# Optimization experiments

Hardware: AMD Instinct MI355X
Metric: run time of the kernel (lower is better)

Reference implementation:

```python
import jax, jax.numpy as jnp
import numpy as np

POOL = 7  # pool_size from init


def _crop_and_resize_one(fm, boxes):
    """TF crop_and_resize semantics for one image.
    fm: [H,W,C] float; boxes: [N,4] normalized x1y1x2y2 (module reorders to y1x1y2x2
    before calling tf.image.crop_and_resize; here we just pick the right coords).
    Returns [N,POOL,POOL,C]."""
    H, W, C = fm.shape
    x1, y1, x2, y2 = boxes[:, 0], boxes[:, 1], boxes[:, 2], boxes[:, 3]
    i = jnp.arange(POOL, dtype=fm.dtype)
    # sample coords per TF: start*(size-1) + i*(end-start)*(size-1)/(POOL-1)
    ys = y1[:, None] * (H - 1) + i[None, :] * ((y2 - y1) * (H - 1) / (POOL - 1))[:, None]  # [N,P]
    xs = x1[:, None] * (W - 1) + i[None, :] * ((x2 - x1) * (W - 1) / (POOL - 1))[:, None]  # [N,P]

    def lerp_idx(v, size):
        v0 = jnp.floor(v)
        frac = v - v0
        i0 = jnp.clip(v0, 0, size - 1).astype(jnp.int32)
        i1 = jnp.clip(v0 + 1, 0, size - 1).astype(jnp.int32)
        valid = (v >= 0) & (v <= size - 1)  # TF extrapolates with 0 outside image
        return i0, i1, frac, valid

    yt, yb, fy, vy = lerp_idx(ys, H)
    xl, xr, fx, vx = lerp_idx(xs, W)
    # gather 4 corners via advanced indexing -> [N,P,P,C]
    tl = fm[yt[:, :, None], xl[:, None, :]]
    tr = fm[yt[:, :, None], xr[:, None, :]]
    bl = fm[yb[:, :, None], xl[:, None, :]]
    br = fm[yb[:, :, None], xr[:, None, :]]
    fy_ = fy[:, :, None, None]
    fx_ = fx[:, None, :, None]
    top = tl + (tr - tl) * fx_
    bot = bl + (br - bl) * fx_
    out = top + (bot - top) * fy_
    mask = (vy[:, :, None] & vx[:, None, :])[..., None]
    return jnp.where(mask, out, jnp.zeros((), fm.dtype))


def setup_inputs() -> dict:
    key = jax.random.key(0)
    k1, k2, k3 = jax.random.split(key, 3)
    B, H, W, C, N = 8, 64, 64, 256, 512
    feature_map = jax.random.normal(k1, (B, H, W, C), dtype=jnp.float32)
    # build valid normalized boxes x1y1x2y2 with x1<=x2, y1<=y2
    p = jax.random.uniform(k2, (B, N, 2), dtype=jnp.float32)
    q = jax.random.uniform(k3, (B, N, 2), dtype=jnp.float32)
    lo = jnp.minimum(p, q)
    hi = jnp.maximum(p, q)
    rpn_pred = jnp.concatenate([lo, hi], axis=-1)  # [B,N,4] x1y1x2y2
    return {"feature_map": feature_map, "rpn_pred": rpn_pred}


def reference(feature_map, rpn_pred):
    # vmap over batch replaces the tf.while_loop over images
    return jax.vmap(_crop_and_resize_one)(feature_map, rpn_pred)  # [B,N,P,P,C]
```

## Files before the change

kernel.cpp:

```cpp
#include <hip/hip_runtime.h>


#define POOL  7
#define B_    8
#define H_    64
#define W_    64
#define C_    256
#define N_    512
#define CW    (C_ / 4)
#define ROWS_PER_IMG (N_ * POOL)
#define ROWS_PER_BLOCK 4

typedef float v4f __attribute__((ext_vector_type(4)));

__global__ __launch_bounds__(256) void roialign_kernel(
    const float* __restrict__ fm,
    const float* __restrict__ boxes,
    float* __restrict__ out)
{
    const int b    = blockIdx.x & 7;
    const int rblk = blockIdx.x >> 3;
    const int wave = threadIdx.x >> 6;
    const int lane = threadIdx.x & 63;
    const int row  = rblk * ROWS_PER_BLOCK + wave;
    const int n    = row / POOL;
    const int py   = row - n * POOL;

    const float* box = boxes + ((b << 9) + n) * 4;
    const float bx1 = box[0], by1 = box[1], bx2 = box[2], by2 = box[3];

    const float sy  = (by2 - by1) * 63.0f / 6.0f;
    const float sx  = (bx2 - bx1) * 63.0f / 6.0f;
    const float yv  = by1 * 63.0f + (float)py * sy;
    const float x0v = bx1 * 63.0f;

    const float yf = floorf(yv);
    const float fy = yv - yf;
    const int   y0 = (int)yf;
    const int   yt = min(max(y0,     0), H_ - 1);
    const int   yb = min(max(y0 + 1, 0), H_ - 1);
    const bool  vy = (yv >= 0.0f) && (yv <= 63.0f);

    const v4f* f4  = (const v4f*)fm;
    const int rowT = (b * (H_ * W_) + yt * W_) * CW + lane;
    const int rowB = (b * (H_ * W_) + yb * W_) * CW + lane;

    v4f* o4 = (v4f*)out + ((((b << 9) + n) * POOL + py) * POOL) * CW + lane;

    #pragma unroll
    for (int px = 0; px < POOL; ++px) {
        const float xv = x0v + (float)px * sx;
        const float xf = floorf(xv);
        const float fx = xv - xf;
        const int   x0 = (int)xf;
        const int   xl = min(max(x0,     0), W_ - 1);
        const int   xr = min(max(x0 + 1, 0), W_ - 1);
        const bool  valid = vy && (xv >= 0.0f) && (xv <= 63.0f);

        const v4f tl = f4[rowT + xl * CW];
        const v4f tr = f4[rowT + xr * CW];
        const v4f bl = f4[rowB + xl * CW];
        const v4f br = f4[rowB + xr * CW];

        const v4f top = tl + (tr - tl) * fx;
        const v4f bot = bl + (br - bl) * fx;
        v4f o = top + (bot - top) * fy;
        if (!valid) o = (v4f)(0.0f);

        __builtin_nontemporal_store(o, o4 + px * CW);
    }
}

extern "C" void kernel_launch(void* const* d_in, const int* in_sizes, int n_in,
                              void* d_out, int out_size, void* d_ws, size_t ws_size,
                              hipStream_t stream) {
    const float* fm    = (const float*)d_in[0];
    const float* boxes = (const float*)d_in[1];
    float* out         = (float*)d_out;

    const int blocks = (ROWS_PER_IMG / ROWS_PER_BLOCK) * B_;

    roialign_kernel<<<blocks, 256, 0, stream>>>(fm, boxes, out);
}
```

Baseline: 246.0 us.

## Sort boxes by y1 per image to improve feature-map cache locality

Adds a per-image bitonic sort of box indices by y1 coordinate in shared memory, then has the RoI-align kernel process boxes in sorted order via a permutation array. Neighbouring blocks then touch similar feature-map rows, with the aim of raising L2/MALL hit rates on the gathers. Output is still written to each box's original slot, so results are unchanged. The cost is an extra small kernel launch, a workspace dependency and a serialized dependent load of the permutation. Writes become scattered by box rather than sequential.

```diff
diff --git a/kernel.cpp b/kernel.cpp
--- a/kernel.cpp
+++ b/kernel.cpp
@@ -13,9 +13,38 @@
 
 typedef float v4f __attribute__((ext_vector_type(4)));
 
+__global__ __launch_bounds__(512) void sort_boxes_kernel(
+    const float* __restrict__ boxes,
+    int* __restrict__ perm)
+{
+    const int b = blockIdx.x;
+    const int t = threadIdx.x;
+    __shared__ float key[N_];
+    __shared__ int   idx[N_];
+    key[t] = boxes[((b << 9) + t) * 4 + 1];
+    idx[t] = t;
+    __syncthreads();
+    for (int k = 2; k <= N_; k <<= 1) {
+        for (int j = k >> 1; j > 0; j >>= 1) {
+            const int ixj = t ^ j;
+            if (ixj > t) {
+                const bool up = ((t & k) == 0);
+                const float a = key[t], c = key[ixj];
+                if (up ? (a > c) : (a < c)) {
+                    key[t] = c; key[ixj] = a;
+                    const int tmp = idx[t]; idx[t] = idx[ixj]; idx[ixj] = tmp;
+                }
+            }
+            __syncthreads();
+        }
+    }
+    perm[(b << 9) + t] = idx[t];
+}
+
 __global__ __launch_bounds__(256) void roialign_kernel(
     const float* __restrict__ fm,
     const float* __restrict__ boxes,
+    const int*  __restrict__ perm,
     float* __restrict__ out)
 {
     const int b    = blockIdx.x & 7;
@@ -23,8 +52,10 @@
     const int wave = threadIdx.x >> 6;
     const int lane = threadIdx.x & 63;
     const int row  = rblk * ROWS_PER_BLOCK + wave;
-    const int n    = row / POOL;
-    const int py   = row - n * POOL;
+    const int ns   = row / POOL;
+    const int py   = row - ns * POOL;
+
+    const int n = __builtin_amdgcn_readfirstlane(perm[(b << 9) + ns]);
 
     const float* box = boxes + ((b << 9) + n) * 4;
     const float bx1 = box[0], by1 = box[1], bx2 = box[2], by2 = box[3];
@@ -77,8 +108,10 @@
     const float* fm    = (const float*)d_in[0];
     const float* boxes = (const float*)d_in[1];
     float* out         = (float*)d_out;
+    int*   perm        = (int*)d_ws;
+
+    sort_boxes_kernel<<<B_, N_, 0, stream>>>(boxes, perm);
 
     const int blocks = (ROWS_PER_IMG / ROWS_PER_BLOCK) * B_;
-
-    roialign_kernel<<<blocks, 256, 0, stream>>>(fm, boxes, out);
+    roialign_kernel<<<blocks, 256, 0, stream>>>(fm, boxes, perm, out);
 }
```

After: 259.1 us. +5.3%, slower.

## Bucket ROI sample rows by feature-map row and serve bilinear taps from LDS

Applied to the files above, without the earlier changes.

Adds a pre-pass kernel that builds, per image, a histogram and prefix sum that group every (box, pool-row) item by the top feature-map row it samples. The main kernel then runs one block per (image, row). Each block stages that row and the row below (128 KB) in LDS and processes all bucketed items, reading the four bilinear corners from LDS instead of global memory. This is meant to remove repeated scattered global/L2 gathers. In exchange it adds a second launch and a serial scan, and drops to 512 blocks with very large LDS use, which limits occupancy. Bucket sizes are uneven, so blocks get unequal work, and the large dynamic LDS request may need hardware and launch support.

```diff
diff --git a/kernel.cpp b/kernel.cpp
--- a/kernel.cpp
+++ b/kernel.cpp
@@ -8,66 +8,129 @@
 #define C_    256
 #define N_    512
 #define CW    (C_ / 4)
-#define ROWS_PER_IMG (N_ * POOL)
-#define ROWS_PER_BLOCK 4
+#define ROWQ  (W_ * CW)
+#define ITEMS_PER_IMG (N_ * POOL)
 
 typedef float v4f __attribute__((ext_vector_type(4)));
+typedef unsigned short u16;
+
+__global__ __launch_bounds__(512) void bucket_kernel(
+    const float* __restrict__ boxes,
+    int* __restrict__ offs,
+    u16* __restrict__ items)
+{
+    const int b = blockIdx.x;
+    const int n = threadIdx.x;
+    __shared__ int hist[H_];
+    __shared__ int base[H_];
+    __shared__ int cnt[H_];
+    if (n < H_) hist[n] = 0;
+    __syncthreads();
+
+    const float by1 = boxes[(((b << 9) + n) << 2) + 1];
+    const float by2 = boxes[(((b << 9) + n) << 2) + 3];
+    const float sy = (by2 - by1) * 63.0f / 6.0f;
+    int bk[POOL];
+    #pragma unroll
+    for (int py = 0; py < POOL; ++py) {
+        const float yv = by1 * 63.0f + (float)py * sy;
+        const int y0 = (int)floorf(yv);
+        bk[py] = min(max(y0, 0), H_ - 1);
+        atomicAdd(&hist[bk[py]], 1);
+    }
+    __syncthreads();
+    if (n == 0) {
+        int run = 0;
+        for (int i = 0; i < H_; ++i) { base[i] = run; run += hist[i]; }
+    }
+    if (n < H_) cnt[n] = 0;
+    __syncthreads();
+    #pragma unroll
+    for (int py = 0; py < POOL; ++py) {
+        const int pos = base[bk[py]] + atomicAdd(&cnt[bk[py]], 1);
+        items[b * ITEMS_PER_IMG + pos] = (u16)((n << 3) | py);
+    }
+    if (n < H_) offs[b * (H_ + 1) + n] = base[n];
+    if (n == 0) offs[b * (H_ + 1) + H_] = ITEMS_PER_IMG;
+}
 
 __global__ __launch_bounds__(256) void roialign_kernel(
     const float* __restrict__ fm,
     const float* __restrict__ boxes,
+    const int*  __restrict__ offs,
+    const u16*  __restrict__ items,
     float* __restrict__ out)
 {
+    extern __shared__ v4f lds[];
     const int b    = blockIdx.x & 7;
-    const int rblk = blockIdx.x >> 3;
-    const int wave = threadIdx.x >> 6;
-    const int lane = threadIdx.x & 63;
-    const int row  = rblk * ROWS_PER_BLOCK + wave;
-    const int n    = row / POOL;
-    const int py   = row - n * POOL;
+    const int bk   = blockIdx.x >> 3;
+    const int tid  = threadIdx.x;
+    const int wave = tid >> 6;
+    const int lane = tid & 63;
+    const v4f* f4  = (const v4f*)fm;
 
-    const float* box = boxes + ((b << 9) + n) * 4;
-    const float bx1 = box[0], by1 = box[1], bx2 = box[2], by2 = box[3];
+    {
+        const int base0 = (b * H_ + bk) * ROWQ;
+        const int base1 = (b * H_ + min(bk + 1, H_ - 1)) * ROWQ;
+        #pragma unroll
+        for (int k = 0; k < 16; ++k)
+            lds[k * 256 + tid] = f4[base0 + k * 256 + tid];
+        #pragma unroll
+        for (int k = 0; k < 16; ++k)
+            lds[ROWQ + k * 256 + tid] = f4[base1 + k * 256 + tid];
+    }
+    __syncthreads();
 
-    const float sy  = (by2 - by1) * 63.0f / 6.0f;
-    const float sx  = (bx2 - bx1) * 63.0f / 6.0f;
-    const float yv  = by1 * 63.0f + (float)py * sy;
-    const float x0v = bx1 * 63.0f;
+    const int start = offs[b * (H_ + 1) + bk];
+    const int end   = offs[b * (H_ + 1) + bk + 1];
 
-    const float yf = floorf(yv);
-    const float fy = yv - yf;
-    const int   y0 = (int)yf;
-    const int   yt = min(max(y0,     0), H_ - 1);
-    const int   yb = min(max(y0 + 1, 0), H_ - 1);
-    const bool  vy = (yv >= 0.0f) && (yv <= 63.0f);
+    for (int it = start + wave; it < end; it += 4) {
+        const int code = __builtin_amdgcn_readfirstlane(
+                             (int)items[b * ITEMS_PER_IMG + it]);
+        const int n  = code >> 3;
+        const int py = code & 7;
 
-    const v4f* f4  = (const v4f*)fm;
-    const int rowT = (b * (H_ * W_) + yt * W_) * CW + lane;
-    const int rowB = (b * (H_ * W_) + yb * W_) * CW + lane;
+        const float* box = boxes + (((b << 9) + n) << 2);
+        const float bx1 = box[0], by1 = box[1], bx2 = box[2], by2 = box[3];
 
-    v4f* o4 = (v4f*)out + ((((b << 9) + n) * POOL + py) * POOL) * CW + lane;
+        const float sy  = (by2 - by1) * 63.0f / 6.0f;
+        const float sx  = (bx2 - bx1) * 63.0f / 6.0f;
+        const float yv  = by1 * 63.0f + (float)py * sy;
+        const float x0v = bx1 * 63.0f;
 
-    #pragma unroll
-    for (int px = 0; px < POOL; ++px) {
-        const float xv = x0v + (float)px * sx;
-        const float xf = floorf(xv);
-        const float fx = xv - xf;
-        const int   x0 = (int)xf;
-        const int   xl = min(max(x0,     0), W_ - 1);
-        const int   xr = min(max(x0 + 1, 0), W_ - 1);
-        const bool  valid = vy && (xv >= 0.0f) && (xv <= 63.0f);
+        const float yf = floorf(yv);
+        const float fy = yv - yf;
+        const int   y0 = (int)yf;
+        const int   yt = min(max(y0,     0), H_ - 1);
+        const int   yb = min(max(y0 + 1, 0), H_ - 1);
+        const bool  vy = (yv >= 0.0f) && (yv <= 63.0f);
 
-        const v4f tl = f4[rowT + xl * CW];
-        const v4f tr = f4[rowT + xr * CW];
-        const v4f bl = f4[rowB + xl * CW];
-        const v4f br = f4[rowB + xr * CW];
+        const int offB = (yb > yt) ? ROWQ : 0;
 
-        const v4f top = tl + (tr - tl) * fx;
-        const v4f bot = bl + (br - bl) * fx;
-        v4f o = top + (bot - top) * fy;
-        if (!valid) o = (v4f)(0.0f);
+        v4f* o4 = (v4f*)out + ((((b << 9) + n) * POOL + py) * POOL) * CW + lane;
 
-        __builtin_nontemporal_store(o, o4 + px * CW);
+        #pragma unroll
+        for (int px = 0; px < POOL; ++px) {
+            const float xv = x0v + (float)px * sx;
+            const float xf = floorf(xv);
+            const float fx = xv - xf;
+            const int   x0 = (int)xf;
+            const int   xl = min(max(x0,     0), W_ - 1);
+            const int   xr = min(max(x0 + 1, 0), W_ - 1);
+            const bool  valid = vy && (xv >= 0.0f) && (xv <= 63.0f);
+
+            const v4f tl = lds[       xl * CW + lane];
+            const v4f tr = lds[       xr * CW + lane];
+            const v4f bl = lds[offB + xl * CW + lane];
+            const v4f br = lds[offB + xr * CW + lane];
+
+            const v4f top = tl + (tr - tl) * fx;
+            const v4f bot = bl + (br - bl) * fx;
+            v4f o = top + (bot - top) * fy;
+            if (!valid) o = (v4f)(0.0f);
+
+            __builtin_nontemporal_store(o, o4 + px * CW);
+        }
     }
 }
 
@@ -78,7 +141,11 @@
     const float* boxes = (const float*)d_in[1];
     float* out         = (float*)d_out;
 
-    const int blocks = (ROWS_PER_IMG / ROWS_PER_BLOCK) * B_;
+    int* offs  = (int*)d_ws;
+    u16* items = (u16*)((char*)d_ws + 4096);
 
-    roialign_kernel<<<blocks, 256, 0, stream>>>(fm, boxes, out);
+    bucket_kernel<<<B_, N_, 0, stream>>>(boxes, offs, items);
+
+    roialign_kernel<<<H_ * B_, 256, 2 * ROWQ * sizeof(v4f), stream>>>(
+        fm, boxes, offs, items, out);
 }
```

Result: no change. 241.8 us (-1.7%).

## Bucket ROI rows by top feature row and stage that row in LDS

Applied to the files above, without the earlier changes.

The kernel now launches one 512-thread block per (image, feature row, parity half). Each block copies its top feature row (64 KB) into LDS, then builds a compacted list of the (box, py) samples whose top row matches, using an LDS atomic counter. Waves walk that list, reading top corners from LDS and bottom corners from global memory. The goal is to cut redundant global gather traffic, at the cost of an extra row load per block, possible load imbalance between rows, and plain stores in place of nontemporal ones.

```diff
diff --git a/kernel.cpp b/kernel.cpp
--- a/kernel.cpp
+++ b/kernel.cpp
@@ -8,66 +8,103 @@
 #define C_    256
 #define N_    512
 #define CW    (C_ / 4)
-#define ROWS_PER_IMG (N_ * POOL)
-#define ROWS_PER_BLOCK 4
+#define ROWQ  (W_ * CW)
+#define MAXI  3584
 
 typedef float v4f __attribute__((ext_vector_type(4)));
+typedef unsigned short u16;
 
-__global__ __launch_bounds__(256) void roialign_kernel(
+__global__ __launch_bounds__(512) void roialign_kernel(
     const float* __restrict__ fm,
     const float* __restrict__ boxes,
     float* __restrict__ out)
 {
+    extern __shared__ v4f lds[];
+    u16* list = (u16*)(lds + ROWQ);
+    __shared__ int cnt;
+
     const int b    = blockIdx.x & 7;
-    const int rblk = blockIdx.x >> 3;
-    const int wave = threadIdx.x >> 6;
-    const int lane = threadIdx.x & 63;
-    const int row  = rblk * ROWS_PER_BLOCK + wave;
-    const int n    = row / POOL;
-    const int py   = row - n * POOL;
+    const int u    = blockIdx.x >> 3;
+    const int bk   = u >> 1;
+    const int half = u & 1;
+    const int tid  = threadIdx.x;
+    const int wave = tid >> 6;
+    const int lane = tid & 63;
+    const v4f* f4  = (const v4f*)fm;
 
-    const float* box = boxes + ((b << 9) + n) * 4;
-    const float bx1 = box[0], by1 = box[1], bx2 = box[2], by2 = box[3];
+    if (tid == 0) cnt = 0;
+    __syncthreads();
 
-    const float sy  = (by2 - by1) * 63.0f / 6.0f;
-    const float sx  = (bx2 - bx1) * 63.0f / 6.0f;
-    const float yv  = by1 * 63.0f + (float)py * sy;
-    const float x0v = bx1 * 63.0f;
+    {
+        const int base0 = (b * H_ + bk) * ROWQ;
+        #pragma unroll
+        for (int k = 0; k < 8; ++k)
+            lds[k * 512 + tid] = f4[base0 + k * 512 + tid];
+    }
 
-    const float yf = floorf(yv);
-    const float fy = yv - yf;
-    const int   y0 = (int)yf;
-    const int   yt = min(max(y0,     0), H_ - 1);
-    const int   yb = min(max(y0 + 1, 0), H_ - 1);
-    const bool  vy = (yv >= 0.0f) && (yv <= 63.0f);
+    {
+        const int n = tid;
+        const float by1 = boxes[(((b << 9) + n) << 2) + 1];
+        const float by2 = boxes[(((b << 9) + n) << 2) + 3];
+        const float sy  = (by2 - by1) * 63.0f / 6.0f;
+        #pragma unroll
+        for (int py = 0; py < POOL; ++py) {
+            const float yv = by1 * 63.0f + (float)py * sy;
+            const int y0  = (int)floorf(yv);
+            const int bkk = min(max(y0, 0), H_ - 1);
+            if (bkk == bk && (((n + py) & 1) == half)) {
+                const int pos = atomicAdd(&cnt, 1);
+                list[pos] = (u16)((n << 3) | py);
+            }
+        }
+    }
+    __syncthreads();
 
-    const v4f* f4  = (const v4f*)fm;
-    const int rowT = (b * (H_ * W_) + yt * W_) * CW + lane;
-    const int rowB = (b * (H_ * W_) + yb * W_) * CW + lane;
+    const int nItems = cnt;
+    const int yb       = min(bk + 1, H_ - 1);
+    const int rowBbase = (b * (H_ * W_) + yb * W_) * CW + lane;
+    const float yfB    = (float)bk;
 
-    v4f* o4 = (v4f*)out + ((((b << 9) + n) * POOL + py) * POOL) * CW + lane;
+    for (int it = wave; it < nItems; it += 8) {
+        const int code = __builtin_amdgcn_readfirstlane((int)list[it]);
+        const int n  = code >> 3;
+        const int py = code & 7;
 
-    #pragma unroll
-    for (int px = 0; px < POOL; ++px) {
-        const float xv = x0v + (float)px * sx;
-        const float xf = floorf(xv);
-        const float fx = xv - xf;
-        const int   x0 = (int)xf;
-        const int   xl = min(max(x0,     0), W_ - 1);
-        const int   xr = min(max(x0 + 1, 0), W_ - 1);
-        const bool  valid = vy && (xv >= 0.0f) && (xv <= 63.0f);
+        const float* box = boxes + (((b << 9) + n) << 2);
+        const float bx1 = box[0], by1 = box[1], bx2 = box[2], by2 = box[3];
 
-        const v4f tl = f4[rowT + xl * CW];
-        const v4f tr = f4[rowT + xr * CW];
-        const v4f bl = f4[rowB + xl * CW];
-        const v4f br = f4[rowB + xr * CW];
+        const float sy  = (by2 - by1) * 63.0f / 6.0f;
+        const float sx  = (bx2 - bx1) * 63.0f / 6.0f;
+        const float yv  = by1 * 63.0f + (float)py * sy;
+        const float x0v = bx1 * 63.0f;
 
-        const v4f top = tl + (tr - tl) * fx;
-        const v4f bot = bl + (br - bl) * fx;
-        v4f o = top + (bot - top) * fy;
-        if (!valid) o = (v4f)(0.0f);
+        const float fy = yv - yfB;
+        const bool  vy = (yv >= 0.0f) && (yv <= 63.0f);
 
-        __builtin_nontemporal_store(o, o4 + px * CW);
+        v4f* o4 = (v4f*)out + ((((b << 9) + n) * POOL + py) * POOL) * CW + lane;
+
+        #pragma unroll
+        for (int px = 0; px < POOL; ++px) {
+            const float xv = x0v + (float)px * sx;
+            const float xf = floorf(xv);
+            const float fx = xv - xf;
+            const int   x0 = (int)xf;
+            const int   xl = min(max(x0,     0), W_ - 1);
+            const int   xr = min(max(x0 + 1, 0), W_ - 1);
+            const bool  valid = vy && (xv >= 0.0f) && (xv <= 63.0f);
+
+            const v4f tl = lds[xl * CW + lane];
+            const v4f tr = lds[xr * CW + lane];
+            const v4f bl = f4[rowBbase + xl * CW];
+            const v4f br = f4[rowBbase + xr * CW];
+
+            const v4f top = tl + (tr - tl) * fx;
+            const v4f bot = bl + (br - bl) * fx;
+            v4f o = top + (bot - top) * fy;
+            if (!valid) o = (v4f)(0.0f);
+
+            o4[px * CW] = o;
+        }
     }
 }
 
@@ -78,7 +115,6 @@
     const float* boxes = (const float*)d_in[1];
     float* out         = (float*)d_out;
 
-    const int blocks = (ROWS_PER_IMG / ROWS_PER_BLOCK) * B_;
-
-    roialign_kernel<<<blocks, 256, 0, stream>>>(fm, boxes, out);
+    const size_t ldsB = ROWQ * sizeof(v4f) + MAXI * sizeof(u16);
+    roialign_kernel<<<H_ * 2 * B_, 512, ldsB, stream>>>(fm, boxes, out);
 }
```

Result: faster. 231.5 us (-5.9%).
